# Performance work log

Hardware: AMD Instinct MI355X
Metric: run time of the kernel (lower is better)

Reference implementation:

```python
import jax, jax.numpy as jnp
import numpy as np

COS_EPS = 1e-8  # torch F.cosine_similarity eps


def setup_inputs() -> dict:
    key = jax.random.key(0)
    k1, k2 = jax.random.split(key)
    N, D = 4096, 1024
    features = jax.random.normal(k1, (N, D), dtype=jnp.float32)
    y = jax.random.randint(k2, (N,), 0, 100, dtype=jnp.int64)
    return {"features": features, "y": y}


def reference(features, y):
    y = y.reshape(-1)
    # shared building blocks: row norms and Gram matrix (one GEMM)
    sq = jnp.sum(features * features, axis=-1)            # [N]
    gram = features @ features.T                           # [N, N]
    # Euclidean cdist via ||a||^2 + ||b||^2 - 2 a.b, safe sqrt (grad 0 at 0)
    d2 = sq[:, None] + sq[None, :] - 2.0 * gram
    pos = d2 > 0
    dist = jnp.where(pos, jnp.sqrt(jnp.where(pos, d2, 1.0)), 0.0)
    # cosine similarity with torch-style eps clamp on norms
    norm = jnp.maximum(jnp.sqrt(sq), COS_EPS)              # [N]
    sim = gram / (norm[:, None] * norm[None, :])
    # (eq - ~eq) = 2*eq - 1 signed mask
    eq = (y[:, None] == y[None, :])
    sgn = jnp.where(eq, 1.0, -1.0).astype(features.dtype)
    # loss = sum(sgn * dist) + sum(-sgn * sim)
    return jnp.sum(sgn * dist) - jnp.sum(sgn * sim)
```

## Files before the change

kernel.cpp:

```cpp
#include <hip/hip_runtime.h>
#include <stdint.h>

typedef __attribute__((ext_vector_type(4)))  int   i32x4;
typedef __attribute__((ext_vector_type(8)))  int   i32x8;
typedef __attribute__((ext_vector_type(16))) float f32x16;

#define NROWS 4096
#define DDIM  1024
#define NKT   16
#define GBLK  256
#define COS_EPS 1e-8f
#define SCL   0x7F7F7F7F

__device__ __forceinline__ void gload16(const uint8_t* g, uint8_t* l) {
  __builtin_amdgcn_global_load_lds(
      (const __attribute__((address_space(1))) uint32_t*)g,
      (__attribute__((address_space(3))) uint32_t*)l, 16, 0, 0);
}

extern "C" __global__ void __launch_bounds__(256) prep_kernel(
    const float* __restrict__ F, uint8_t* __restrict__ Fb,
    float* __restrict__ sq, float* __restrict__ rn) {
  const int row  = blockIdx.x * 4 + (threadIdx.x >> 6);
  const int lane = threadIdx.x & 63;
  const float4* src = (const float4*)(F + (size_t)row * DDIM + lane * 16);
  float4 v[4];
#pragma unroll
  for (int i = 0; i < 4; ++i) v[i] = src[i];
  float s = 0.f;
#pragma unroll
  for (int i = 0; i < 4; ++i)
    s += v[i].x * v[i].x + v[i].y * v[i].y + v[i].z * v[i].z + v[i].w * v[i].w;
  uint32_t d[4];
#pragma unroll
  for (int i = 0; i < 4; ++i) {
    int w = __builtin_amdgcn_cvt_pk_fp8_f32(v[i].x, v[i].y, 0, false);
    w = __builtin_amdgcn_cvt_pk_fp8_f32(v[i].z, v[i].w, w, true);
    d[i] = (uint32_t)w;
  }
  *(uint4*)(Fb + (size_t)row * DDIM + lane * 16) = make_uint4(d[0], d[1], d[2], d[3]);
#pragma unroll
  for (int off = 32; off; off >>= 1) s += __shfl_down(s, off);
  if (lane == 0) {
    sq[row] = s;
    rn[row] = 1.0f / fmaxf(sqrtf(s), COS_EPS);
  }
}

extern "C" __global__ void __launch_bounds__(512, 1) gram_kernel(
    const uint8_t* __restrict__ Fb, const float* __restrict__ sq,
    const float* __restrict__ rn, const int* __restrict__ y,
    float* __restrict__ partials) {
  __shared__ __align__(16) uint8_t As[4][16384];
  __shared__ __align__(16) uint8_t Bs[4][16384];

  const int wg = (int)(blockIdx.x & 7) * 32 + (int)(blockIdx.x >> 3);
  const int bi = wg >> 4, bj = wg & 15;

  const int tid  = threadIdx.x;
  const int lane = tid & 63;
  const int wid  = tid >> 6;
  const int wr   = wid >> 2;
  const int wc   = wid & 3;
  const int kg   = lane >> 5;
  const int r32  = lane & 31;

  const int u7 = (tid >> 3) & 7;
  const int hc = (tid & 7) ^ u7;
  const int srow = 2 * (tid >> 3) + ((hc >> 2) & 1);
  const int scol = (hc & 3) * 16;
  const uint8_t* gA0 = Fb + (size_t)(bi * 256 + srow) * DDIM + scol;
  const uint8_t* gB0 = Fb + (size_t)(bj * 256 + srow) * DDIM + scol;
  uint8_t* ldsA = &As[0][0] + tid * 16;
  uint8_t* ldsB = &Bs[0][0] + tid * 16;

  int offA[4], offB[2];
#pragma unroll
  for (int mt = 0; mt < 4; ++mt) {
    const int R = wr * 128 + mt * 32 + r32;
    const int u = R >> 1, h = R & 1;
    offA[mt] = u * 128 + (((h << 2) + 2 * kg) ^ (u & 7)) * 16;
  }
#pragma unroll
  for (int nb = 0; nb < 2; ++nb) {
    const int R = wc * 64 + nb * 32 + r32;
    const int u = R >> 1, h = R & 1;
    offB[nb] = u * 128 + (((h << 2) + 2 * kg) ^ (u & 7)) * 16;
  }

  f32x16 acc[4][2] = {};

#define STAGE(kt2) do {                                                     \
    const int _sl = (kt2) & 3;                                              \
    gload16(gA0 + (kt2) * 64, ldsA + _sl * 16384);                          \
    gload16(gA0 + (size_t)128 * DDIM + (kt2) * 64, ldsA + _sl * 16384 + 8192); \
    gload16(gB0 + (kt2) * 64, ldsB + _sl * 16384);                          \
    gload16(gB0 + (size_t)128 * DDIM + (kt2) * 64, ldsB + _sl * 16384 + 8192); \
  } while (0)

#define LDF(dst, base, off) do {                                            \
    i32x4 _lo = *(const i32x4*)((base) + (off));                            \
    i32x4 _hi = *(const i32x4*)((base) + ((off) ^ 16));                     \
    dst[0] = _lo[0]; dst[1] = _lo[1]; dst[2] = _lo[2]; dst[3] = _lo[3];     \
    dst[4] = _hi[0]; dst[5] = _hi[1]; dst[6] = _hi[2]; dst[7] = _hi[3];     \
  } while (0)

#define MM(mt, nb, a, b)                                                    \
    acc[mt][nb] = __builtin_amdgcn_mfma_scale_f32_32x32x64_f8f6f4(          \
        a, b, acc[mt][nb], 0, 0, 0, SCL, 0, SCL)

  STAGE(0); STAGE(1);
  asm volatile("s_waitcnt vmcnt(4)");
  __builtin_amdgcn_s_barrier();

#pragma unroll 1
  for (int kt = 0; kt < NKT; ++kt) {
    const uint8_t* sa = &As[0][0] + (kt & 3) * 16384;
    const uint8_t* sb = &Bs[0][0] + (kt & 3) * 16384;
    i32x8 a0, a1, a2, a3, b0, b1;

    LDF(b0, sb, offB[0]); LDF(b1, sb, offB[1]);
    LDF(a0, sa, offA[0]); LDF(a1, sa, offA[1]);
    if (kt + 2 < NKT) {
      const int _sl = (kt + 2) & 3;
      gload16(gA0 + (kt + 2) * 64, ldsA + _sl * 16384);
      gload16(gA0 + (size_t)128 * DDIM + (kt + 2) * 64, ldsA + _sl * 16384 + 8192);
    }
    __builtin_amdgcn_s_barrier();
    __builtin_amdgcn_s_setprio(1);
    MM(0, 0, a0, b0); MM(0, 1, a0, b1);
    MM(1, 0, a1, b0); MM(1, 1, a1, b1);
    __builtin_amdgcn_s_setprio(0);
    __builtin_amdgcn_s_barrier();

    LDF(a2, sa, offA[2]); LDF(a3, sa, offA[3]);
    if (kt + 2 < NKT) {
      const int _sl = (kt + 2) & 3;
      gload16(gB0 + (kt + 2) * 64, ldsB + _sl * 16384);
      gload16(gB0 + (size_t)128 * DDIM + (kt + 2) * 64, ldsB + _sl * 16384 + 8192);
    }
    if (kt < NKT - 2)       asm volatile("s_waitcnt vmcnt(4)");
    else if (kt == NKT - 2) asm volatile("s_waitcnt vmcnt(0)");
    __builtin_amdgcn_s_barrier();
    __builtin_amdgcn_s_setprio(1);
    MM(2, 0, a2, b0); MM(2, 1, a2, b1);
    MM(3, 0, a3, b0); MM(3, 1, a3, b1);
    __builtin_amdgcn_s_setprio(0);
    __builtin_amdgcn_s_barrier();
  }

#undef STAGE
#undef LDF
#undef MM

  float sqc[2], rnc[2];
  int   yc[2];
#pragma unroll
  for (int nb = 0; nb < 2; ++nb) {
    const int gj = bj * 256 + wc * 64 + nb * 32 + r32;
    sqc[nb] = sq[gj]; rnc[nb] = rn[gj]; yc[nb] = y[gj];
  }
  float lsum = 0.f;
#pragma unroll
  for (int mt = 0; mt < 4; ++mt) {
#pragma unroll
    for (int e = 0; e < 16; ++e) {
      const int gi = bi * 256 + wr * 128 + mt * 32 + (e & 3) + 8 * (e >> 2) + 4 * kg;
      const float sqi = sq[gi], rni = rn[gi];
      const int yi = y[gi];
#pragma unroll
      for (int nb = 0; nb < 2; ++nb) {
        const float g  = acc[mt][nb][e];
        const float d2 = sqi + sqc[nb] - 2.0f * g;
        const float dist = d2 > 0.f ? sqrtf(d2) : 0.f;
        const float sim  = g * rni * rnc[nb];
        lsum += (yi == yc[nb]) ? (dist - sim) : (sim - dist);
      }
    }
  }
#pragma unroll
  for (int off = 32; off; off >>= 1) lsum += __shfl_down(lsum, off);
  __shared__ float wsum[8];
  if (lane == 0) wsum[wid] = lsum;
  __syncthreads();
  if (tid == 0) {
    float t = 0.f;
#pragma unroll
    for (int i = 0; i < 8; ++i) t += wsum[i];
    partials[blockIdx.x] = t;
  }
}

extern "C" __global__ void __launch_bounds__(256) reduce_kernel(
    const float* __restrict__ partials, float* __restrict__ out) {
  float s = 0.f;
  for (int i = threadIdx.x; i < GBLK; i += 256) s += partials[i];
#pragma unroll
  for (int off = 32; off; off >>= 1) s += __shfl_down(s, off);
  __shared__ float ws[4];
  if ((threadIdx.x & 63) == 0) ws[threadIdx.x >> 6] = s;
  __syncthreads();
  if (threadIdx.x == 0) out[0] = ws[0] + ws[1] + ws[2] + ws[3];
}

extern "C" void kernel_launch(void* const* d_in, const int* in_sizes, int n_in,
                              void* d_out, int out_size, void* d_ws, size_t ws_size,
                              hipStream_t stream) {
  const float* F = (const float*)d_in[0];
  const int*   y = (const int*)d_in[1];
  float* out = (float*)d_out;

  uint8_t* Fb = (uint8_t*)d_ws;
  float*  sq = (float*)((char*)d_ws + (size_t)NROWS * DDIM);
  float*  rn = sq + NROWS;
  float*  partials = rn + NROWS;

  prep_kernel<<<NROWS / 4, 256, 0, stream>>>(F, Fb, sq, rn);
  gram_kernel<<<GBLK, 512, 0, stream>>>(Fb, sq, rn, y, partials);
  reduce_kernel<<<1, 256, 0, stream>>>(partials, out);
}
```

Measured before the change: 41.46 us.

## Shrink gram tiles to 256x128 with 3-stage buffering for higher occupancy

Halves the B tile width so the grid grows to 512 workgroups, and each wave now owns a 64x64 output block (2x2 MFMAs) instead of 128x64. The LDS ring drops from 4 to 3 stages with a smaller B buffer, and launch bounds allow several blocks per CU, so more waves can hide latency. The per-iteration schedule is simplified to one load phase, one MFMA phase and one barrier, with sched_barriers added. The cost is that each B tile feeds fewer MFMAs, so there is more global and LDS traffic per unit of compute, and the pipeline now has one barrier per k-step.

```diff
diff --git a/kernel.cpp b/kernel.cpp
--- a/kernel.cpp
+++ b/kernel.cpp
@@ -8,7 +8,7 @@
 #define NROWS 4096
 #define DDIM  1024
 #define NKT   16
-#define GBLK  256
+#define GBLK  512
 #define COS_EPS 1e-8f
 #define SCL   0x7F7F7F7F
 
@@ -16,6 +16,13 @@
   __builtin_amdgcn_global_load_lds(
       (const __attribute__((address_space(1))) uint32_t*)g,
       (__attribute__((address_space(3))) uint32_t*)l, 16, 0, 0);
+}
+
+__device__ __forceinline__ i32x8 cat8(i32x4 lo, i32x4 hi) {
+  i32x8 r;
+  r[0] = lo[0]; r[1] = lo[1]; r[2] = lo[2]; r[3] = lo[3];
+  r[4] = hi[0]; r[5] = hi[1]; r[6] = hi[2]; r[7] = hi[3];
+  return r;
 }
 
 extern "C" __global__ void __launch_bounds__(256) prep_kernel(
@@ -47,37 +54,37 @@
   }
 }
 
-extern "C" __global__ void __launch_bounds__(512, 1) gram_kernel(
+extern "C" __global__ void __launch_bounds__(512, 4) gram_kernel(
     const uint8_t* __restrict__ Fb, const float* __restrict__ sq,
     const float* __restrict__ rn, const int* __restrict__ y,
     float* __restrict__ partials) {
-  __shared__ __align__(16) uint8_t As[4][16384];
-  __shared__ __align__(16) uint8_t Bs[4][16384];
-
-  const int wg = (int)(blockIdx.x & 7) * 32 + (int)(blockIdx.x >> 3);
-  const int bi = wg >> 4, bj = wg & 15;
+  __shared__ __align__(16) uint8_t As[3][16384];
+  __shared__ __align__(16) uint8_t Bs[3][8192];
+
+  const int wg = (int)(blockIdx.x & 7) * 64 + (int)(blockIdx.x >> 3);
+  const int bi = wg >> 5, bj = wg & 31;
 
   const int tid  = threadIdx.x;
   const int lane = tid & 63;
   const int wid  = tid >> 6;
-  const int wr   = wid >> 2;
-  const int wc   = wid & 3;
+  const int wr   = wid >> 1;
+  const int wc   = wid & 1;
   const int kg   = lane >> 5;
   const int r32  = lane & 31;
 
-  const int u7 = (tid >> 3) & 7;
-  const int hc = (tid & 7) ^ u7;
+  const int hc   = (tid & 7) ^ ((tid >> 3) & 7);
   const int srow = 2 * (tid >> 3) + ((hc >> 2) & 1);
   const int scol = (hc & 3) * 16;
   const uint8_t* gA0 = Fb + (size_t)(bi * 256 + srow) * DDIM + scol;
-  const uint8_t* gB0 = Fb + (size_t)(bj * 256 + srow) * DDIM + scol;
+  const uint8_t* gA1 = gA0 + (size_t)128 * DDIM;
+  const uint8_t* gB0 = Fb + (size_t)(bj * 128 + srow) * DDIM + scol;
   uint8_t* ldsA = &As[0][0] + tid * 16;
   uint8_t* ldsB = &Bs[0][0] + tid * 16;
 
-  int offA[4], offB[2];
-#pragma unroll
-  for (int mt = 0; mt < 4; ++mt) {
-    const int R = wr * 128 + mt * 32 + r32;
+  int offA[2], offB[2];
+#pragma unroll
+  for (int mt = 0; mt < 2; ++mt) {
+    const int R = wr * 64 + mt * 32 + r32;
     const int u = R >> 1, h = R & 1;
     offA[mt] = u * 128 + (((h << 2) + 2 * kg) ^ (u & 7)) * 16;
   }
@@ -88,84 +95,73 @@
     offB[nb] = u * 128 + (((h << 2) + 2 * kg) ^ (u & 7)) * 16;
   }
 
-  f32x16 acc[4][2] = {};
+  f32x16 acc[2][2] = {};
 
 #define STAGE(kt2) do {                                                     \
-    const int _sl = (kt2) & 3;                                              \
+    const int _sl = (kt2) % 3;                                              \
     gload16(gA0 + (kt2) * 64, ldsA + _sl * 16384);                          \
-    gload16(gA0 + (size_t)128 * DDIM + (kt2) * 64, ldsA + _sl * 16384 + 8192); \
-    gload16(gB0 + (kt2) * 64, ldsB + _sl * 16384);                          \
-    gload16(gB0 + (size_t)128 * DDIM + (kt2) * 64, ldsB + _sl * 16384 + 8192); \
+    gload16(gA1 + (kt2) * 64, ldsA + _sl * 16384 + 8192);                   \
+    gload16(gB0 + (kt2) * 64, ldsB + _sl * 8192);                           \
   } while (0)
 
-#define LDF(dst, base, off) do {                                            \
-    i32x4 _lo = *(const i32x4*)((base) + (off));                            \
-    i32x4 _hi = *(const i32x4*)((base) + ((off) ^ 16));                     \
-    dst[0] = _lo[0]; dst[1] = _lo[1]; dst[2] = _lo[2]; dst[3] = _lo[3];     \
-    dst[4] = _hi[0]; dst[5] = _hi[1]; dst[6] = _hi[2]; dst[7] = _hi[3];     \
-  } while (0)
-
-#define MM(mt, nb, a, b)                                                    \
-    acc[mt][nb] = __builtin_amdgcn_mfma_scale_f32_32x32x64_f8f6f4(          \
-        a, b, acc[mt][nb], 0, 0, 0, SCL, 0, SCL)
-
   STAGE(0); STAGE(1);
-  asm volatile("s_waitcnt vmcnt(4)");
+  asm volatile("s_waitcnt vmcnt(3)");
   __builtin_amdgcn_s_barrier();
+  __builtin_amdgcn_sched_barrier(0);
 
 #pragma unroll 1
   for (int kt = 0; kt < NKT; ++kt) {
-    const uint8_t* sa = &As[0][0] + (kt & 3) * 16384;
-    const uint8_t* sb = &Bs[0][0] + (kt & 3) * 16384;
-    i32x8 a0, a1, a2, a3, b0, b1;
-
-    LDF(b0, sb, offB[0]); LDF(b1, sb, offB[1]);
-    LDF(a0, sa, offA[0]); LDF(a1, sa, offA[1]);
+    const uint8_t* sa = &As[0][0] + (kt % 3) * 16384;
+    const uint8_t* sb = &Bs[0][0] + (kt % 3) * 8192;
+
+    i32x4 a0l = *(const i32x4*)(sa + offA[0]);
+    i32x4 a1l = *(const i32x4*)(sa + offA[1]);
+    i32x4 b0l = *(const i32x4*)(sb + offB[0]);
+    i32x4 b1l = *(const i32x4*)(sb + offB[1]);
+    i32x4 a0h = *(const i32x4*)(sa + (offA[0] ^ 16));
+    i32x4 a1h = *(const i32x4*)(sa + (offA[1] ^ 16));
+    i32x4 b0h = *(const i32x4*)(sb + (offB[0] ^ 16));
+    i32x4 b1h = *(const i32x4*)(sb + (offB[1] ^ 16));
+
     if (kt + 2 < NKT) {
-      const int _sl = (kt + 2) & 3;
-      gload16(gA0 + (kt + 2) * 64, ldsA + _sl * 16384);
-      gload16(gA0 + (size_t)128 * DDIM + (kt + 2) * 64, ldsA + _sl * 16384 + 8192);
+      STAGE(kt + 2);
+      asm volatile("s_waitcnt vmcnt(3)");
+    } else {
+      asm volatile("s_waitcnt vmcnt(0)");
     }
+
+    const i32x8 A0 = cat8(a0l, a0h), A1 = cat8(a1l, a1h);
+    const i32x8 B0 = cat8(b0l, b0h), B1 = cat8(b1l, b1h);
+    __builtin_amdgcn_s_setprio(1);
+    acc[0][0] = __builtin_amdgcn_mfma_scale_f32_32x32x64_f8f6f4(
+        A0, B0, acc[0][0], 0, 0, 0, SCL, 0, SCL);
+    acc[0][1] = __builtin_amdgcn_mfma_scale_f32_32x32x64_f8f6f4(
+        A0, B1, acc[0][1], 0, 0, 0, SCL, 0, SCL);
+    acc[1][0] = __builtin_amdgcn_mfma_scale_f32_32x32x64_f8f6f4(
+        A1, B0, acc[1][0], 0, 0, 0, SCL, 0, SCL);
+    acc[1][1] = __builtin_amdgcn_mfma_scale_f32_32x32x64_f8f6f4(
+        A1, B1, acc[1][1], 0, 0, 0, SCL, 0, SCL);
+    __builtin_amdgcn_s_setprio(0);
+
     __builtin_amdgcn_s_barrier();
-    __builtin_amdgcn_s_setprio(1);
-    MM(0, 0, a0, b0); MM(0, 1, a0, b1);
-    MM(1, 0, a1, b0); MM(1, 1, a1, b1);
-    __builtin_amdgcn_s_setprio(0);
-    __builtin_amdgcn_s_barrier();
-
-    LDF(a2, sa, offA[2]); LDF(a3, sa, offA[3]);
-    if (kt + 2 < NKT) {
-      const int _sl = (kt + 2) & 3;
-      gload16(gB0 + (kt + 2) * 64, ldsB + _sl * 16384);
-      gload16(gB0 + (size_t)128 * DDIM + (kt + 2) * 64, ldsB + _sl * 16384 + 8192);
-    }
-    if (kt < NKT - 2)       asm volatile("s_waitcnt vmcnt(4)");
-    else if (kt == NKT - 2) asm volatile("s_waitcnt vmcnt(0)");
-    __builtin_amdgcn_s_barrier();
-    __builtin_amdgcn_s_setprio(1);
-    MM(2, 0, a2, b0); MM(2, 1, a2, b1);
-    MM(3, 0, a3, b0); MM(3, 1, a3, b1);
-    __builtin_amdgcn_s_setprio(0);
-    __builtin_amdgcn_s_barrier();
+    __builtin_amdgcn_sched_barrier(0);
   }
 
 #undef STAGE
-#undef LDF
-#undef MM
 
   float sqc[2], rnc[2];
   int   yc[2];
 #pragma unroll
   for (int nb = 0; nb < 2; ++nb) {
-    const int gj = bj * 256 + wc * 64 + nb * 32 + r32;
+    const int gj = bj * 128 + wc * 64 + nb * 32 + r32;
     sqc[nb] = sq[gj]; rnc[nb] = rn[gj]; yc[nb] = y[gj];
   }
   float lsum = 0.f;
 #pragma unroll
-  for (int mt = 0; mt < 4; ++mt) {
+  for (int mt = 0; mt < 2; ++mt) {
 #pragma unroll
     for (int e = 0; e < 16; ++e) {
-      const int gi = bi * 256 + wr * 128 + mt * 32 + (e & 3) + 8 * (e >> 2) + 4 * kg;
+      const int gi = bi * 256 + wr * 64 + mt * 32 + (e & 3) + 8 * (e >> 2) + 4 * kg;
       const float sqi = sq[gi], rni = rn[gi];
       const int yi = y[gi];
 #pragma unroll
```

After: 44.05 us. 6.2% more time.
